# Kernel optimization log

Measured on AMD Instinct MI355X. Metric: run time of the kernel, lower is better.

## Reference

```python
import math
import jax, jax.numpy as jnp
import numpy as np

B, T, D = 4, 4096, 1024
H = 16            # n_heads
HD = D // H       # head_dim = 64
CAP = int(4096 * 0.125)  # mod capacity k = 512
DFF = int(D * 4 * 2 / 3)  # 2730, per SwiGLU
EPS = 1e-6


def rmsnorm(x, g):
    return x * jax.lax.rsqrt(jnp.mean(x * x, axis=-1, keepdims=True) + EPS) * g


def setup_inputs() -> dict:
    key = jax.random.key(0)
    ks = jax.random.split(key, 9)
    s = lambda k, shape: (jax.random.normal(k, shape, jnp.float32) * 0.02)
    return {
        "x": jax.random.normal(ks[0], (B, T, D), jnp.float32),
        "w_router": s(ks[1], (D,)),          # router Linear(d_model,1,bias=False)
        "W_qkv": s(ks[2], (3 * D, D)),       # torch Linear weight layout [out,in]
        "W_out": s(ks[3], (D, D)),
        "g1": jnp.ones((D,), jnp.float32),   # RMSNorm weights
        "g2": jnp.ones((D,), jnp.float32),
        "W1": s(ks[4], (DFF, D)),
        "W2": s(ks[5], (DFF, D)),
        "W3": s(ks[6], (D, DFF)),
    }


def reference(x, w_router, W_qkv, W_out, g1, g2, W1, W2, W3):
    Bq, Tq, Dq = x.shape
    # --- MoD routing: top-k tokens per sequence (T > capacity) ---
    scores = x @ w_router                         # [B, T]
    _, idx = jax.lax.top_k(scores, CAP)           # [B, k], descending-score order (matches torch.topk)
    x_sel = jnp.take_along_axis(x, idx[:, :, None], axis=1)  # [B, k, D]

    # --- causal attention on the gathered subset ---
    h = rmsnorm(x_sel, g1)
    qkv = (h @ W_qkv.T).reshape(Bq, CAP, 3, H, HD)
    q, k, v = jnp.moveaxis(qkv, 2, 0)             # each [B, k, H, HD]
    att = jnp.einsum('bqhd,bkhd->bhqk', q, k) / math.sqrt(HD)
    mask = jnp.triu(jnp.ones((CAP, CAP), bool), 1)  # causal mask in gathered order
    att = jnp.where(mask, -jnp.inf, att)
    att = jax.nn.softmax(att, axis=-1)
    o = jnp.einsum('bhqk,bkhd->bqhd', att, v).reshape(Bq, CAP, Dq)
    x_attn = o @ W_out.T

    # --- SwiGLU FFN ---
    h2 = rmsnorm(x_sel + x_attn, g2)
    x_ff = (jax.nn.silu(h2 @ W1.T) * (h2 @ W2.T)) @ W3.T

    # --- combine and scatter back into the full sequence ---
    x_proc = x_sel + x_attn + x_ff                # [B, k, D]
    out = x.at[jnp.arange(Bq)[:, None], idx].set(x_proc)
    return out
```

## Files before the change

kernel.cpp:

```cpp
#include <hip/hip_runtime.h>
#include <hip/hip_bf16.h>


#define B_   4
#define T_   4096
#define D_   1024
#define H_   16
#define HD_  64
#define CAP_ 512
#define DFF_ 2730
#define DFFP 2752
#define DFFR 2816
#define M_   (B_*CAP_)

typedef __attribute__((ext_vector_type(8))) short          s16x8;
typedef __attribute__((ext_vector_type(8))) unsigned short u16x8;
typedef __attribute__((ext_vector_type(4))) float          f32x4;

__device__ __forceinline__ float bf2f(unsigned short u) {
    union { float f; unsigned int i; } v; v.i = ((unsigned int)u) << 16; return v.f;
}
__device__ __forceinline__ unsigned short f2bf(float f) {
    union { float f; unsigned int i; } v; v.f = f;
    unsigned int r = v.i + 0x7fffu + ((v.i >> 16) & 1u);
    return (unsigned short)(r >> 16);
}

__device__ __forceinline__ void gload_lds16(const unsigned short* g, unsigned short* l) {
    __builtin_amdgcn_global_load_lds(
        (const __attribute__((address_space(1))) unsigned int*)g,
        (__attribute__((address_space(3))) unsigned int*)l, 16, 0, 0);
}

__global__ __launch_bounds__(256) void k_copy_router(const float* __restrict__ x,
                                                     const float* __restrict__ wr,
                                                     float* __restrict__ out,
                                                     float* __restrict__ sc) {
    int gw   = (blockIdx.x * 256 + threadIdx.x) >> 6;
    int lane = threadIdx.x & 63;
    const float* row = x + (size_t)gw * D_;
    float* orow = out + (size_t)gw * D_;
    float s = 0.f;
#pragma unroll
    for (int p = 0; p < 4; ++p) {
        int c = p * 256 + lane * 4;
        float4 xv = *(const float4*)(row + c);
        float4 wv = *(const float4*)(wr + c);
        *(float4*)(orow + c) = xv;
        s += xv.x * wv.x + xv.y * wv.y + xv.z * wv.z + xv.w * wv.w;
    }
#pragma unroll
    for (int o = 32; o; o >>= 1) s += __shfl_xor(s, o);
    if (lane == 0) sc[gw] = s;
}

__global__ __launch_bounds__(256) void k_f2b(const float4* __restrict__ s,
                                             ushort4* __restrict__ d, int n4) {
    int i = blockIdx.x * 256 + threadIdx.x;
    int st = gridDim.x * 256;
    for (; i < n4; i += st) {
        float4 v = s[i];
        ushort4 o;
        o.x = f2bf(v.x); o.y = f2bf(v.y); o.z = f2bf(v.z); o.w = f2bf(v.w);
        d[i] = o;
    }
}

__global__ __launch_bounds__(256) void k_f2b_rowpad2(const float* __restrict__ s1,
                                                     const float* __restrict__ s2,
                                                     unsigned short* __restrict__ d1,
                                                     unsigned short* __restrict__ d2,
                                                     int kc, int rows, int total) {
    int g = blockIdx.x * 256 + threadIdx.x;
    int st = gridDim.x * 256;
    for (; g < total; g += st) {
        int row = g / kc;
        u16x8 v1 = {0,0,0,0,0,0,0,0}, v2 = {0,0,0,0,0,0,0,0};
        if (row < rows) {
            const float* p1 = s1 + ((size_t)g) * 8;
            const float* p2 = s2 + ((size_t)g) * 8;
#pragma unroll
            for (int j = 0; j < 2; ++j) {
                float4 f1 = *(const float4*)(p1 + 4 * j);
                float4 f2 = *(const float4*)(p2 + 4 * j);
                v1[4*j] = f2bf(f1.x); v1[4*j+1] = f2bf(f1.y);
                v1[4*j+2] = f2bf(f1.z); v1[4*j+3] = f2bf(f1.w);
                v2[4*j] = f2bf(f2.x); v2[4*j+1] = f2bf(f2.y);
                v2[4*j+2] = f2bf(f2.z); v2[4*j+3] = f2bf(f2.w);
            }
        }
        *(u16x8*)(d1 + (size_t)g * 8) = v1;
        *(u16x8*)(d2 + (size_t)g * 8) = v2;
    }
}

__global__ __launch_bounds__(256) void k_f2b_pad(const float* __restrict__ src,
                                                 unsigned short* __restrict__ dst,
                                                 int K, int Kp, int rows) {
    int g = blockIdx.x * 256 + threadIdx.x;
    int ng = rows * (Kp >> 3);
    int st = gridDim.x * 256;
    for (; g < ng; g += st) {
        int row = g / (Kp >> 3);
        int c = (g - row * (Kp >> 3)) << 3;
        const float* s = src + (size_t)row * K + c;
        u16x8 v;
        if (c + 8 <= K) {
#pragma unroll
            for (int j = 0; j < 4; ++j) {
                float2 f = *(const float2*)(s + 2 * j);
                v[2*j] = f2bf(f.x); v[2*j+1] = f2bf(f.y);
            }
        } else {
#pragma unroll
            for (int j = 0; j < 8; ++j) v[j] = (c + j < K) ? f2bf(s[j]) : (unsigned short)0;
        }
        *(u16x8*)(dst + (size_t)row * Kp + c) = v;
    }
}

__global__ __launch_bounds__(1024) void k_topk(const float* __restrict__ sc,
                                               int* __restrict__ idx) {
    __shared__ unsigned int hist[256];
    __shared__ unsigned long long okeys[CAP_];
    __shared__ unsigned int ecand[T_];
    __shared__ unsigned int sprefix;
    __shared__ int skneed;
    __shared__ unsigned int scnt, ecnt;
    int t = threadIdx.x;
    const float* s = sc + (size_t)blockIdx.x * T_;

    unsigned int sb[4], ei[4];
#pragma unroll
    for (int j = 0; j < 4; ++j) {
        int i = j * 1024 + t;
        union { float f; unsigned int u; } v; v.f = s[i];
        unsigned int k = (v.u & 0x80000000u) ? ~v.u : (v.u | 0x80000000u);
        sb[j] = ~k;
        ei[j] = (unsigned int)i;
    }
    if (t == 0) { sprefix = 0; skneed = CAP_; scnt = 0; ecnt = 0; }

#pragma unroll
    for (int rs = 24; rs >= 0; rs -= 8) {
        if (t < 256) hist[t] = 0;
        __syncthreads();
        unsigned int pfx = sprefix;
#pragma unroll
        for (int j = 0; j < 4; ++j) {
            if (((unsigned long long)(sb[j] ^ pfx) >> (rs + 8)) == 0ULL)
                atomicAdd(&hist[(sb[j] >> rs) & 255u], 1u);
        }
        __syncthreads();
        if (t < 64) {
            unsigned int h0 = hist[t * 4], h1 = hist[t * 4 + 1];
            unsigned int h2 = hist[t * 4 + 2], h3 = hist[t * 4 + 3];
            unsigned int lsum = h0 + h1 + h2 + h3;
            unsigned int run = lsum;
#pragma unroll
            for (int d = 1; d < 64; d <<= 1) {
                unsigned int v = __shfl_up(run, d);
                if (t >= d) run += v;
            }
            unsigned int excl = run - lsum;
            int need = skneed;
            if (excl < (unsigned int)need && run >= (unsigned int)need) {
                unsigned int cum = excl;
                int b = t * 4;
                if (cum + h0 < (unsigned int)need) { cum += h0; ++b;
                    if (cum + h1 < (unsigned int)need) { cum += h1; ++b;
                        if (cum + h2 < (unsigned int)need) { cum += h2; ++b; } } }
                sprefix = pfx | ((unsigned int)b << rs);
                skneed = need - (int)cum;
            }
        }
        __syncthreads();
    }

    unsigned int Sstar = sprefix;
    int neq = skneed;
#pragma unroll
    for (int j = 0; j < 4; ++j) {
        if (sb[j] < Sstar) {
            unsigned int p = atomicAdd(&scnt, 1u);
            okeys[p] = ((unsigned long long)sb[j] << 32) | ei[j];
        } else if (sb[j] == Sstar) {
            unsigned int p = atomicAdd(&ecnt, 1u);
            ecand[p] = ei[j];
        }
    }
    __syncthreads();
    if (t == 0) {
        unsigned int base = scnt;
        unsigned int ne = ecnt;
        for (int q = 0; q < neq; ++q) {
            unsigned int mn = 0xffffffffu; int mi = 0;
            for (unsigned int e = 0; e < ne; ++e)
                if (ecand[e] < mn) { mn = ecand[e]; mi = (int)e; }
            okeys[base + q] = ((unsigned long long)Sstar << 32) | mn;
            ecand[mi] = 0xffffffffu;
        }
    }
    __syncthreads();
    if (t < CAP_) {
        unsigned long long mine = okeys[t];
        int r = 0;
#pragma unroll 8
        for (int q = 0; q < CAP_; ++q) r += (okeys[q] < mine) ? 1 : 0;
        idx[blockIdx.x * CAP_ + r] = (int)(mine & 0xffffffffu);
    }
}

__global__ __launch_bounds__(256) void k_gather_rms(const float* __restrict__ x,
                                                    const int* __restrict__ idx,
                                                    const float* __restrict__ g,
                                                    unsigned short* __restrict__ h) {
    int r = blockIdx.x;
    int b = r >> 9;
    int src = idx[r] & (T_ - 1);
    const float* xr = x + ((size_t)b * T_ + src) * D_;
    int c = threadIdx.x * 4;
    float4 xv = *(const float4*)(xr + c);
    float ss = xv.x*xv.x + xv.y*xv.y + xv.z*xv.z + xv.w*xv.w;
#pragma unroll
    for (int o = 32; o; o >>= 1) ss += __shfl_xor(ss, o);
    __shared__ float red[4];
    int lane = threadIdx.x & 63, w = threadIdx.x >> 6;
    if (lane == 0) red[w] = ss;
    __syncthreads();
    float tot = red[0] + red[1] + red[2] + red[3];
    float scale = rsqrtf(tot * (1.f / D_) + 1e-6f);
    float4 gv = *(const float4*)(g + c);
    ushort4 hv;
    hv.x = f2bf(xv.x * scale * gv.x);
    hv.y = f2bf(xv.y * scale * gv.y);
    hv.z = f2bf(xv.z * scale * gv.z);
    hv.w = f2bf(xv.w * scale * gv.w);
    *(ushort4*)(h + (size_t)r * D_ + c) = hv;
}

__global__ __launch_bounds__(512) void k_gemm128g(const unsigned short* __restrict__ A,
                                                  const unsigned short* __restrict__ Bw,
                                                  unsigned short* __restrict__ C,
                                                  int Nout, int Kr) {
    __shared__ __align__(16) unsigned short As[2][128 * 64];
    __shared__ __align__(16) unsigned short Bs[2][128 * 64];
    int m0 = blockIdx.x * 128;
    int n0 = blockIdx.y * 128;
    int t = threadIdx.x;
    int w = t >> 6, lane = t & 63;
    int lr = lane & 15, lg = lane >> 4;
    int l8 = lane >> 3, lm8 = lane & 7;
    int wm = (w >> 2) * 64, wn = (w & 3) * 32;

    int srow = w * 16 + l8;
    int cb0 = lm8 ^ (srow & 7), cb1 = lm8 ^ ((srow + 8) & 7);

    f32x4 acc[4][2];
#pragma unroll
    for (int mi = 0; mi < 4; ++mi)
#pragma unroll
        for (int ni = 0; ni < 2; ++ni) acc[mi][ni] = {0.f, 0.f, 0.f, 0.f};

#define STAGE_128(buf, k0)                                                        \
    {                                                                             \
        gload_lds16(A + (size_t)(m0 + srow) * Kr + (k0) + cb0 * 8,                \
                    &As[buf][(w * 16) * 64]);                                     \
        gload_lds16(A + (size_t)(m0 + srow + 8) * Kr + (k0) + cb1 * 8,            \
                    &As[buf][(w * 16 + 8) * 64]);                                 \
        gload_lds16(Bw + (size_t)(n0 + srow) * Kr + (k0) + cb0 * 8,               \
                    &Bs[buf][(w * 16) * 64]);                                     \
        gload_lds16(Bw + (size_t)(n0 + srow + 8) * Kr + (k0) + cb1 * 8,           \
                    &Bs[buf][(w * 16 + 8) * 64]);                                 \
    }

    int nk = Kr >> 6;
    STAGE_128(0, 0);
    __syncthreads();
    for (int kt = 0; kt < nk; ++kt) {
        int cur = kt & 1;
        if (kt + 1 < nk) STAGE_128(cur ^ 1, (kt + 1) << 6);
#pragma unroll
        for (int kh = 0; kh < 2; ++kh) {
            s16x8 af[4], bf[2];
#pragma unroll
            for (int i = 0; i < 4; ++i) {
                int row = wm + i * 16 + lr;
                int pb = (kh * 4 + lg) ^ (row & 7);
                af[i] = *(const s16x8*)&As[cur][row * 64 + pb * 8];
            }
#pragma unroll
            for (int i = 0; i < 2; ++i) {
                int row = wn + i * 16 + lr;
                int pb = (kh * 4 + lg) ^ (row & 7);
                bf[i] = *(const s16x8*)&Bs[cur][row * 64 + pb * 8];
            }
#pragma unroll
            for (int mi = 0; mi < 4; ++mi)
#pragma unroll
                for (int ni = 0; ni < 2; ++ni)
                    acc[mi][ni] = __builtin_amdgcn_mfma_f32_16x16x32_bf16(af[mi], bf[ni],
                                                                          acc[mi][ni], 0, 0, 0);
        }
        __syncthreads();
    }
#undef STAGE_128
    int orow0 = m0 + wm + (lg << 2);
    int ocol0 = n0 + wn + lr;
#pragma unroll
    for (int ni = 0; ni < 2; ++ni) {
        int col = ocol0 + ni * 16;
        if (col < Nout) {
#pragma unroll
            for (int mi = 0; mi < 4; ++mi)
#pragma unroll
                for (int i = 0; i < 4; ++i)
                    C[(size_t)(orow0 + mi * 16 + i) * Nout + col] = f2bf(acc[mi][ni][i]);
        }
    }
}

template<int EPI>
__global__ __launch_bounds__(512) void k_gemm64g(const unsigned short* __restrict__ A,
                                                 const unsigned short* __restrict__ Bw,
                                                 unsigned short* __restrict__ C,
                                                 int Nout, int Kr,
                                                 const unsigned short* __restrict__ Y,
                                                 const int* __restrict__ idxp,
                                                 float* __restrict__ outp) {
    __shared__ __align__(16) unsigned short As[3][64 * 64];
    __shared__ __align__(16) unsigned short Bs[3][128 * 64];
    int m0 = blockIdx.x * 64;
    int n0 = blockIdx.y * 128;
    int t = threadIdx.x;
    int w = t >> 6, lane = t & 63;
    int lr = lane & 15, lg = lane >> 4;
    int l8 = lane >> 3, lm8 = lane & 7;

    int arow = w * 8 + l8;
    int acb  = lm8 ^ (arow & 7);
    int brow = w * 16 + l8;
    int bcb0 = lm8 ^ (brow & 7), bcb1 = lm8 ^ ((brow + 8) & 7);

    f32x4 acc[4];
#pragma unroll
    for (int mi = 0; mi < 4; ++mi) acc[mi] = {0.f, 0.f, 0.f, 0.f};

#define STAGE_G(buf, k0)                                                          \
    {                                                                             \
        gload_lds16(A + (size_t)(m0 + arow) * Kr + (k0) + acb * 8,                \
                    &As[buf][(w * 8) * 64]);                                      \
        gload_lds16(Bw + (size_t)(n0 + brow) * Kr + (k0) + bcb0 * 8,              \
                    &Bs[buf][(w * 16) * 64]);                                     \
        gload_lds16(Bw + (size_t)(n0 + brow + 8) * Kr + (k0) + bcb1 * 8,          \
                    &Bs[buf][(w * 16 + 8) * 64]);                                 \
    }

    int nk = Kr >> 6;
    STAGE_G(0, 0);
    STAGE_G(1, 64);
    asm volatile("s_waitcnt vmcnt(3)" ::: "memory");
    __builtin_amdgcn_s_barrier();
    for (int kt = 0; kt < nk; ++kt) {
        int cur = kt % 3;
        bool more = (kt + 2 < nk);
        if (more) STAGE_G((kt + 2) % 3, (kt + 2) << 6);
#pragma unroll
        for (int kh = 0; kh < 2; ++kh) {
            s16x8 af[4], bf;
#pragma unroll
            for (int i = 0; i < 4; ++i) {
                int row = i * 16 + lr;
                int pb = (kh * 4 + lg) ^ (row & 7);
                af[i] = *(const s16x8*)&As[cur][row * 64 + pb * 8];
            }
            {
                int row = w * 16 + lr;
                int pb = (kh * 4 + lg) ^ (row & 7);
                bf = *(const s16x8*)&Bs[cur][row * 64 + pb * 8];
            }
#pragma unroll
            for (int mi = 0; mi < 4; ++mi)
                acc[mi] = __builtin_amdgcn_mfma_f32_16x16x32_bf16(af[mi], bf, acc[mi], 0, 0, 0);
        }
        if (kt + 1 < nk) {
            if (more) asm volatile("s_waitcnt vmcnt(3)" ::: "memory");
            else      asm volatile("s_waitcnt vmcnt(0)" ::: "memory");
            __builtin_amdgcn_s_barrier();
        }
    }
#undef STAGE_G
    int orow0 = m0 + (lg << 2);
    int col = n0 + w * 16 + lr;
    if (col < Nout) {
#pragma unroll
        for (int mi = 0; mi < 4; ++mi)
#pragma unroll
            for (int i = 0; i < 4; ++i) {
                int r = orow0 + mi * 16 + i;
                if (EPI == 2) {
                    int b = r >> 9;
                    int dst = idxp[r] & (T_ - 1);
                    float yv = bf2f(Y[(size_t)r * D_ + col]);
                    outp[((size_t)(b * T_ + dst)) * D_ + col] = yv + acc[mi][i];
                } else {
                    C[(size_t)r * Nout + col] = f2bf(acc[mi][i]);
                }
            }
    }
}

__global__ __launch_bounds__(512) void k_gemm64g2(const unsigned short* __restrict__ A,
                                                  const unsigned short* __restrict__ B1,
                                                  const unsigned short* __restrict__ B2,
                                                  unsigned short* __restrict__ F,
                                                  int Nout, int Kr) {
    __shared__ __align__(16) unsigned short As[2][64 * 64];
    __shared__ __align__(16) unsigned short B1s[2][128 * 64];
    __shared__ __align__(16) unsigned short B2s[2][128 * 64];
    int m0 = blockIdx.x * 64;
    int n0 = blockIdx.y * 128;
    int t = threadIdx.x;
    int w = t >> 6, lane = t & 63;
    int lr = lane & 15, lg = lane >> 4;
    int l8 = lane >> 3, lm8 = lane & 7;

    int arow = w * 8 + l8;
    int acb  = lm8 ^ (arow & 7);
    int brow = w * 16 + l8;
    int bcb0 = lm8 ^ (brow & 7), bcb1 = lm8 ^ ((brow + 8) & 7);

    f32x4 accU[4], accG[4];
#pragma unroll
    for (int mi = 0; mi < 4; ++mi) {
        accU[mi] = {0.f, 0.f, 0.f, 0.f};
        accG[mi] = {0.f, 0.f, 0.f, 0.f};
    }

#define STAGE_G2(buf, k0)                                                          \
    {                                                                              \
        gload_lds16(A + (size_t)(m0 + arow) * Kr + (k0) + acb * 8,                 \
                    &As[buf][(w * 8) * 64]);                                       \
        size_t go0 = (size_t)(n0 + brow) * Kr + (k0) + bcb0 * 8;                   \
        size_t go1 = (size_t)(n0 + brow + 8) * Kr + (k0) + bcb1 * 8;               \
        gload_lds16(B1 + go0, &B1s[buf][(w * 16) * 64]);                           \
        gload_lds16(B1 + go1, &B1s[buf][(w * 16 + 8) * 64]);                       \
        gload_lds16(B2 + go0, &B2s[buf][(w * 16) * 64]);                           \
        gload_lds16(B2 + go1, &B2s[buf][(w * 16 + 8) * 64]);                       \
    }

    int nk = Kr >> 6;
    STAGE_G2(0, 0);
    __syncthreads();
    for (int kt = 0; kt < nk; ++kt) {
        int cur = kt & 1;
        if (kt + 1 < nk) STAGE_G2(cur ^ 1, (kt + 1) << 6);
#pragma unroll
        for (int kh = 0; kh < 2; ++kh) {
            s16x8 af[4], b1f, b2f;
#pragma unroll
            for (int i = 0; i < 4; ++i) {
                int row = i * 16 + lr;
                int pb = (kh * 4 + lg) ^ (row & 7);
                af[i] = *(const s16x8*)&As[cur][row * 64 + pb * 8];
            }
            {
                int row = w * 16 + lr;
                int pb = (kh * 4 + lg) ^ (row & 7);
                b1f = *(const s16x8*)&B1s[cur][row * 64 + pb * 8];
                b2f = *(const s16x8*)&B2s[cur][row * 64 + pb * 8];
            }
#pragma unroll
            for (int mi = 0; mi < 4; ++mi) {
                accU[mi] = __builtin_amdgcn_mfma_f32_16x16x32_bf16(af[mi], b1f, accU[mi], 0, 0, 0);
                accG[mi] = __builtin_amdgcn_mfma_f32_16x16x32_bf16(af[mi], b2f, accG[mi], 0, 0, 0);
            }
        }
        __syncthreads();
    }
#undef STAGE_G2
    int orow0 = m0 + (lg << 2);
    int col = n0 + w * 16 + lr;
    if (col < Nout) {
#pragma unroll
        for (int mi = 0; mi < 4; ++mi)
#pragma unroll
            for (int i = 0; i < 4; ++i) {
                float u = accU[mi][i];
                float sl = u / (1.f + __expf(-u));
                F[(size_t)(orow0 + mi * 16 + i) * Nout + col] = f2bf(sl * accG[mi][i]);
            }
    }
}

__global__ __launch_bounds__(256) void k_attn_mfma(const unsigned short* __restrict__ qkv,
                                                   unsigned short* __restrict__ o) {
    __shared__ __align__(16) unsigned short Ks[64][72];
    __shared__ __align__(16) unsigned short Vt[64][72];
    __shared__ __align__(16) unsigned short Ps[4][16][72];
    int i_ = blockIdx.x;
    int qt = 7 - (i_ >> 6), h = i_ & 15, b = (i_ >> 4) & 3;
    int q0 = qt * 64;
    int t = threadIdx.x, w = t >> 6, lane = t & 63;
    int lr = lane & 15, lg = lane >> 4;
    const unsigned short* base = qkv + (size_t)b * CAP_ * 3 * D_;

    int qrow = q0 + w * 16 + lr;
    const unsigned short* qp = base + (size_t)qrow * 3 * D_ + h * 64;
    s16x8 aq0 = *(const s16x8*)(qp + lg * 8);
    s16x8 aq1 = *(const s16x8*)(qp + 32 + lg * 8);

    f32x4 zero = {0.f, 0.f, 0.f, 0.f};
    f32x4 oacc[4] = {zero, zero, zero, zero};
    float m_[4], l_[4];
#pragma unroll
    for (int i = 0; i < 4; ++i) { m_[i] = -3.0e38f; l_[i] = 0.f; }

    int qbase = q0 + w * 16 + lg * 4;
    int ntile = qt + 1;

    int skv = t >> 2, sc = (t & 3) * 16;
    for (int kt = 0; kt < ntile; ++kt) {
        int kv0 = kt << 6;
        {
            const unsigned short* kr = base + (size_t)(kv0 + skv) * 3 * D_ + D_     + h * 64 + sc;
            const unsigned short* vr = base + (size_t)(kv0 + skv) * 3 * D_ + 2 * D_ + h * 64 + sc;
            *(u16x8*)&Ks[skv][sc]     = *(const u16x8*)kr;
            *(u16x8*)&Ks[skv][sc + 8] = *(const u16x8*)(kr + 8);
            u16x8 v0 = *(const u16x8*)vr;
            u16x8 v1 = *(const u16x8*)(vr + 8);
#pragma unroll
            for (int j = 0; j < 8; ++j) {
                Vt[sc + j][skv]     = v0[j];
                Vt[sc + 8 + j][skv] = v1[j];
            }
        }
        __syncthreads();
        f32x4 s_[4] = {zero, zero, zero, zero};
#pragma unroll
        for (int qi = 0; qi < 4; ++qi) {
            s16x8 k0 = *(const s16x8*)&Ks[qi * 16 + lr][lg * 8];
            s16x8 k1 = *(const s16x8*)&Ks[qi * 16 + lr][32 + lg * 8];
            s_[qi] = __builtin_amdgcn_mfma_f32_16x16x32_bf16(aq0, k0, s_[qi], 0, 0, 0);
            s_[qi] = __builtin_amdgcn_mfma_f32_16x16x32_bf16(aq1, k1, s_[qi], 0, 0, 0);
        }
#pragma unroll
        for (int qi = 0; qi < 4; ++qi)
#pragma unroll
            for (int i = 0; i < 4; ++i) {
                float v = s_[qi][i] * 0.125f;
                if (kv0 + qi * 16 + lr > qbase + i) v = -3.0e38f;
                s_[qi][i] = v;
            }
        float pm[4];
#pragma unroll
        for (int i = 0; i < 4; ++i)
            pm[i] = fmaxf(fmaxf(s_[0][i], s_[1][i]), fmaxf(s_[2][i], s_[3][i]));
#pragma unroll
        for (int d = 1; d < 16; d <<= 1) {
#pragma unroll
            for (int i = 0; i < 4; ++i) pm[i] = fmaxf(pm[i], __shfl_xor(pm[i], d));
        }
        float p[4][4], ps[4], scl[4];
#pragma unroll
        for (int i = 0; i < 4; ++i) {
            float mn = fmaxf(m_[i], pm[i]);
            scl[i] = __expf(m_[i] - mn);
            ps[i] = 0.f;
#pragma unroll
            for (int qi = 0; qi < 4; ++qi) {
                p[qi][i] = __expf(s_[qi][i] - mn);
                ps[i] += p[qi][i];
            }
            m_[i] = mn;
        }
#pragma unroll
        for (int d = 1; d < 16; d <<= 1) {
#pragma unroll
            for (int i = 0; i < 4; ++i) ps[i] += __shfl_xor(ps[i], d);
        }
#pragma unroll
        for (int i = 0; i < 4; ++i) l_[i] = l_[i] * scl[i] + ps[i];
#pragma unroll
        for (int dg = 0; dg < 4; ++dg)
#pragma unroll
            for (int i = 0; i < 4; ++i) oacc[dg][i] *= scl[i];
#pragma unroll
        for (int qi = 0; qi < 4; ++qi)
#pragma unroll
            for (int i = 0; i < 4; ++i)
                Ps[w][lg * 4 + i][qi * 16 + lr] = f2bf(p[qi][i]);
        __syncthreads();
        s16x8 pa0 = *(const s16x8*)&Ps[w][lr][lg * 8];
        s16x8 pa1 = *(const s16x8*)&Ps[w][lr][32 + lg * 8];
#pragma unroll
        for (int dg = 0; dg < 4; ++dg) {
            s16x8 vf0 = *(const s16x8*)&Vt[dg * 16 + lr][lg * 8];
            s16x8 vf1 = *(const s16x8*)&Vt[dg * 16 + lr][32 + lg * 8];
            oacc[dg] = __builtin_amdgcn_mfma_f32_16x16x32_bf16(pa0, vf0, oacc[dg], 0, 0, 0);
            oacc[dg] = __builtin_amdgcn_mfma_f32_16x16x32_bf16(pa1, vf1, oacc[dg], 0, 0, 0);
        }
        __syncthreads();
    }
    unsigned short* orow = o + ((size_t)(b * CAP_ + qbase)) * D_ + h * 64;
#pragma unroll
    for (int i = 0; i < 4; ++i) {
        float inv = 1.f / l_[i];
#pragma unroll
        for (int dg = 0; dg < 4; ++dg)
            orow[(size_t)i * D_ + dg * 16 + lr] = f2bf(oacc[dg][i] * inv);
    }
}

__global__ __launch_bounds__(256) void k_add_rms(const float* __restrict__ x,
                                                 const int* __restrict__ idx,
                                                 const unsigned short* __restrict__ xattn,
                                                 const float* __restrict__ g,
                                                 unsigned short* __restrict__ y,
                                                 unsigned short* __restrict__ h) {
    int r = blockIdx.x;
    int b = r >> 9;
    int src = idx[r] & (T_ - 1);
    int c = threadIdx.x * 4;
    const float* xr = x + ((size_t)b * T_ + src) * D_;
    float4 xv = *(const float4*)(xr + c);
    size_t off = (size_t)r * D_ + c;
    ushort4 a4 = *(const ushort4*)(xattn + off);
    float v0 = xv.x + bf2f(a4.x);
    float v1 = xv.y + bf2f(a4.y);
    float v2 = xv.z + bf2f(a4.z);
    float v3 = xv.w + bf2f(a4.w);
    float ss = v0*v0 + v1*v1 + v2*v2 + v3*v3;
#pragma unroll
    for (int o = 32; o; o >>= 1) ss += __shfl_xor(ss, o);
    __shared__ float red[4];
    int lane = threadIdx.x & 63, w = threadIdx.x >> 6;
    if (lane == 0) red[w] = ss;
    __syncthreads();
    float tot = red[0] + red[1] + red[2] + red[3];
    float scale = rsqrtf(tot * (1.f / D_) + 1e-6f);
    ushort4 yv;
    yv.x = f2bf(v0); yv.y = f2bf(v1); yv.z = f2bf(v2); yv.w = f2bf(v3);
    *(ushort4*)(y + off) = yv;
    float4 gv = *(const float4*)(g + c);
    ushort4 hv;
    hv.x = f2bf(v0 * scale * gv.x);
    hv.y = f2bf(v1 * scale * gv.y);
    hv.z = f2bf(v2 * scale * gv.z);
    hv.w = f2bf(v3 * scale * gv.w);
    *(ushort4*)(h + off) = hv;
}

extern "C" void kernel_launch(void* const* d_in, const int* in_sizes, int n_in,
                              void* d_out, int out_size, void* d_ws, size_t ws_size,
                              hipStream_t stream) {
    const float* x     = (const float*)d_in[0];
    const float* w_rt  = (const float*)d_in[1];
    const float* W_qkv = (const float*)d_in[2];
    const float* W_out = (const float*)d_in[3];
    const float* g1    = (const float*)d_in[4];
    const float* g2    = (const float*)d_in[5];
    const float* W1    = (const float*)d_in[6];
    const float* W2    = (const float*)d_in[7];
    const float* W3    = (const float*)d_in[8];
    float* out = (float*)d_out;

    char* p = (char*)d_ws;
    float* scores = (float*)p;
    int*   idx    = (int*)(p + 65536);
    size_t off = 131072;
    const size_t WPAD = (size_t)DFFR * D_;
    unsigned short* WBIG = (unsigned short*)(p + off); off += 2 * WPAD * 2;
    unsigned short* WB2  = WBIG + WPAD;
    unsigned short* R1   = (unsigned short*)(p + off); off += (size_t)M_*3*D_*2;
    unsigned short* R2   = (unsigned short*)(p + off); off += (size_t)M_*D_*2;
    unsigned short* R3   = (unsigned short*)(p + off); off += (size_t)M_*D_*2;
    unsigned short* R4   = (unsigned short*)(p + off); off += (size_t)M_*D_*2;

    unsigned short* h1    = R2;
    unsigned short* qkvb  = R1;
    unsigned short* attno = R2;
    unsigned short* xattn = R3;
    unsigned short* ybuf  = R4;
    unsigned short* h2b   = R2;
    unsigned short* fbuf  = R1;

    k_copy_router<<<(B_*T_) / 4, 256, 0, stream>>>(x, w_rt, out, scores);
    k_topk<<<B_, 1024, 0, stream>>>(scores, idx);
    k_gather_rms<<<M_, 256, 0, stream>>>(x, idx, g1, h1);
    k_f2b<<<2048, 256, 0, stream>>>((const float4*)W_qkv, (ushort4*)WBIG, (3*D_*D_) / 4);
    k_gemm128g<<<dim3(M_/128, 3*D_/128), 512, 0, stream>>>(h1, WBIG, qkvb, 3*D_, D_);
    k_attn_mfma<<<dim3((CAP_/64) * H_ * B_), 256, 0, stream>>>(qkvb, attno);
    k_f2b<<<1024, 256, 0, stream>>>((const float4*)W_out, (ushort4*)WBIG, (D_*D_) / 4);
    k_gemm64g<0><<<dim3(M_/64, D_/128), 512, 0, stream>>>(attno, WBIG, xattn, D_, D_,
                                                          nullptr, nullptr, nullptr);
    k_add_rms<<<M_, 256, 0, stream>>>(x, idx, xattn, g2, ybuf, h2b);
    k_f2b_rowpad2<<<2048, 256, 0, stream>>>(W1, W2, WBIG, WB2, D_/8, DFF_,
                                            DFFR*(D_/8));
    k_gemm64g2<<<dim3(M_/64, DFFR/128), 512, 0, stream>>>(h2b, WBIG, WB2, fbuf,
                                                          DFFP, D_);
    k_f2b_pad<<<2048, 256, 0, stream>>>(W3, WBIG, DFF_, DFFP, D_);
    k_gemm64g<2><<<dim3(M_/64, D_/128), 512, 0, stream>>>(fbuf, WBIG, nullptr, D_, DFFP,
                                                          ybuf, idx, out);
}
```

Baseline: 192.0 us.

## Interleave W1/W2 rows and reuse single-B GEMM with fused SwiGLU epilogue

W1 and W2 are converted into one row-interleaved bf16 matrix, so the gate and up projections become a single GEMM over 2*DFFR columns. The SwiGLU combine now happens in the epilogue by swapping adjacent columns between lanes. This removes the dedicated dual-B GEMM kernel and its extra LDS footprint, which should let the generic kernel reach higher occupancy. The down-projection K dimension is padded to 2816 instead of 2752, which adds some wasted MFMA work and bandwidth in the last GEMM.

```diff
diff --git a/kernel.cpp b/kernel.cpp
--- a/kernel.cpp
+++ b/kernel.cpp
@@ -9,7 +9,6 @@
 #define HD_  64
 #define CAP_ 512
 #define DFF_ 2730
-#define DFFP 2752
 #define DFFR 2816
 #define M_   (B_*CAP_)
 
@@ -66,31 +65,27 @@
     }
 }
 
-__global__ __launch_bounds__(256) void k_f2b_rowpad2(const float* __restrict__ s1,
-                                                     const float* __restrict__ s2,
-                                                     unsigned short* __restrict__ d1,
-                                                     unsigned short* __restrict__ d2,
-                                                     int kc, int rows, int total) {
+__global__ __launch_bounds__(256) void k_f2b_ilv(const float* __restrict__ s1,
+                                                 const float* __restrict__ s2,
+                                                 unsigned short* __restrict__ dst,
+                                                 int kc, int rows, int total) {
     int g = blockIdx.x * 256 + threadIdx.x;
     int st = gridDim.x * 256;
     for (; g < total; g += st) {
-        int row = g / kc;
-        u16x8 v1 = {0,0,0,0,0,0,0,0}, v2 = {0,0,0,0,0,0,0,0};
-        if (row < rows) {
-            const float* p1 = s1 + ((size_t)g) * 8;
-            const float* p2 = s2 + ((size_t)g) * 8;
+        int orow = g / kc;
+        int c = (g - orow * kc) << 3;
+        int srow = orow >> 1;
+        u16x8 v = {0,0,0,0,0,0,0,0};
+        if (srow < rows) {
+            const float* s = ((orow & 1) ? s2 : s1) + (size_t)srow * (kc << 3) + c;
 #pragma unroll
             for (int j = 0; j < 2; ++j) {
-                float4 f1 = *(const float4*)(p1 + 4 * j);
-                float4 f2 = *(const float4*)(p2 + 4 * j);
-                v1[4*j] = f2bf(f1.x); v1[4*j+1] = f2bf(f1.y);
-                v1[4*j+2] = f2bf(f1.z); v1[4*j+3] = f2bf(f1.w);
-                v2[4*j] = f2bf(f2.x); v2[4*j+1] = f2bf(f2.y);
-                v2[4*j+2] = f2bf(f2.z); v2[4*j+3] = f2bf(f2.w);
-            }
-        }
-        *(u16x8*)(d1 + (size_t)g * 8) = v1;
-        *(u16x8*)(d2 + (size_t)g * 8) = v2;
+                float4 f = *(const float4*)(s + 4 * j);
+                v[4*j]   = f2bf(f.x); v[4*j+1] = f2bf(f.y);
+                v[4*j+2] = f2bf(f.z); v[4*j+3] = f2bf(f.w);
+            }
+        }
+        *(u16x8*)(dst + (size_t)g * 8) = v;
     }
 }
 
@@ -403,92 +398,16 @@
                     int dst = idxp[r] & (T_ - 1);
                     float yv = bf2f(Y[(size_t)r * D_ + col]);
                     outp[((size_t)(b * T_ + dst)) * D_ + col] = yv + acc[mi][i];
+                } else if (EPI == 1) {
+                    float mine = acc[mi][i];
+                    float other = __shfl_xor(mine, 1);
+                    if (!(lane & 1)) {
+                        float sl = mine / (1.f + __expf(-mine));
+                        C[(size_t)r * DFFR + (col >> 1)] = f2bf(sl * other);
+                    }
                 } else {
                     C[(size_t)r * Nout + col] = f2bf(acc[mi][i]);
                 }
-            }
-    }
-}
-
-__global__ __launch_bounds__(512) void k_gemm64g2(const unsigned short* __restrict__ A,
-                                                  const unsigned short* __restrict__ B1,
-                                                  const unsigned short* __restrict__ B2,
-                                                  unsigned short* __restrict__ F,
-                                                  int Nout, int Kr) {
-    __shared__ __align__(16) unsigned short As[2][64 * 64];
-    __shared__ __align__(16) unsigned short B1s[2][128 * 64];
-    __shared__ __align__(16) unsigned short B2s[2][128 * 64];
-    int m0 = blockIdx.x * 64;
-    int n0 = blockIdx.y * 128;
-    int t = threadIdx.x;
-    int w = t >> 6, lane = t & 63;
-    int lr = lane & 15, lg = lane >> 4;
-    int l8 = lane >> 3, lm8 = lane & 7;
-
-    int arow = w * 8 + l8;
-    int acb  = lm8 ^ (arow & 7);
-    int brow = w * 16 + l8;
-    int bcb0 = lm8 ^ (brow & 7), bcb1 = lm8 ^ ((brow + 8) & 7);
-
-    f32x4 accU[4], accG[4];
-#pragma unroll
-    for (int mi = 0; mi < 4; ++mi) {
-        accU[mi] = {0.f, 0.f, 0.f, 0.f};
-        accG[mi] = {0.f, 0.f, 0.f, 0.f};
-    }
-
-#define STAGE_G2(buf, k0)                                                          \
-    {                                                                              \
-        gload_lds16(A + (size_t)(m0 + arow) * Kr + (k0) + acb * 8,                 \
-                    &As[buf][(w * 8) * 64]);                                       \
-        size_t go0 = (size_t)(n0 + brow) * Kr + (k0) + bcb0 * 8;                   \
-        size_t go1 = (size_t)(n0 + brow + 8) * Kr + (k0) + bcb1 * 8;               \
-        gload_lds16(B1 + go0, &B1s[buf][(w * 16) * 64]);                           \
-        gload_lds16(B1 + go1, &B1s[buf][(w * 16 + 8) * 64]);                       \
-        gload_lds16(B2 + go0, &B2s[buf][(w * 16) * 64]);                           \
-        gload_lds16(B2 + go1, &B2s[buf][(w * 16 + 8) * 64]);                       \
-    }
-
-    int nk = Kr >> 6;
-    STAGE_G2(0, 0);
-    __syncthreads();
-    for (int kt = 0; kt < nk; ++kt) {
-        int cur = kt & 1;
-        if (kt + 1 < nk) STAGE_G2(cur ^ 1, (kt + 1) << 6);
-#pragma unroll
-        for (int kh = 0; kh < 2; ++kh) {
-            s16x8 af[4], b1f, b2f;
-#pragma unroll
-            for (int i = 0; i < 4; ++i) {
-                int row = i * 16 + lr;
-                int pb = (kh * 4 + lg) ^ (row & 7);
-                af[i] = *(const s16x8*)&As[cur][row * 64 + pb * 8];
-            }
-            {
-                int row = w * 16 + lr;
-                int pb = (kh * 4 + lg) ^ (row & 7);
-                b1f = *(const s16x8*)&B1s[cur][row * 64 + pb * 8];
-                b2f = *(const s16x8*)&B2s[cur][row * 64 + pb * 8];
-            }
-#pragma unroll
-            for (int mi = 0; mi < 4; ++mi) {
-                accU[mi] = __builtin_amdgcn_mfma_f32_16x16x32_bf16(af[mi], b1f, accU[mi], 0, 0, 0);
-                accG[mi] = __builtin_amdgcn_mfma_f32_16x16x32_bf16(af[mi], b2f, accG[mi], 0, 0, 0);
-            }
-        }
-        __syncthreads();
-    }
-#undef STAGE_G2
-    int orow0 = m0 + (lg << 2);
-    int col = n0 + w * 16 + lr;
-    if (col < Nout) {
-#pragma unroll
-        for (int mi = 0; mi < 4; ++mi)
-#pragma unroll
-            for (int i = 0; i < 4; ++i) {
-                float u = accU[mi][i];
-                float sl = u / (1.f + __expf(-u));
-                F[(size_t)(orow0 + mi * 16 + i) * Nout + col] = f2bf(sl * accG[mi][i]);
             }
     }
 }
@@ -671,7 +590,6 @@
     size_t off = 131072;
     const size_t WPAD = (size_t)DFFR * D_;
     unsigned short* WBIG = (unsigned short*)(p + off); off += 2 * WPAD * 2;
-    unsigned short* WB2  = WBIG + WPAD;
     unsigned short* R1   = (unsigned short*)(p + off); off += (size_t)M_*3*D_*2;
     unsigned short* R2   = (unsigned short*)(p + off); off += (size_t)M_*D_*2;
     unsigned short* R3   = (unsigned short*)(p + off); off += (size_t)M_*D_*2;
@@ -695,11 +613,11 @@
     k_gemm64g<0><<<dim3(M_/64, D_/128), 512, 0, stream>>>(attno, WBIG, xattn, D_, D_,
                                                           nullptr, nullptr, nullptr);
     k_add_rms<<<M_, 256, 0, stream>>>(x, idx, xattn, g2, ybuf, h2b);
-    k_f2b_rowpad2<<<2048, 256, 0, stream>>>(W1, W2, WBIG, WB2, D_/8, DFF_,
-                                            DFFR*(D_/8));
-    k_gemm64g2<<<dim3(M_/64, DFFR/128), 512, 0, stream>>>(h2b, WBIG, WB2, fbuf,
-                                                          DFFP, D_);
-    k_f2b_pad<<<2048, 256, 0, stream>>>(W3, WBIG, DFF_, DFFP, D_);
-    k_gemm64g<2><<<dim3(M_/64, D_/128), 512, 0, stream>>>(fbuf, WBIG, nullptr, D_, DFFP,
+    k_f2b_ilv<<<2048, 256, 0, stream>>>(W1, W2, WBIG, D_/8, DFF_, 2*DFFR*(D_/8));
+    k_gemm64g<1><<<dim3(M_/64, (2*DFFR)/128), 512, 0, stream>>>(h2b, WBIG, fbuf,
+                                                                2*DFFR, D_,
+                                                                nullptr, nullptr, nullptr);
+    k_f2b_pad<<<2048, 256, 0, stream>>>(W3, WBIG, DFF_, DFFR, D_);
+    k_gemm64g<2><<<dim3(M_/64, D_/128), 512, 0, stream>>>(fbuf, WBIG, nullptr, D_, DFFR,
                                                           ybuf, idx, out);
 }
```

Measured after the change: 202.8 us. 1.06x slower.
